# Kernel optimization log

Measured on AMD Instinct MI355X. Metric: run time of the kernel, lower is better.

The kernel has to match this reference:

```python
import jax, jax.numpy as jnp
import numpy as np

C_IN = 5
KERNEL = 4
DEPTH = 4
C = C_IN + 3  # original + time + 2 CNN channels


def conv1d(x, w, b):
    # x: (B, Cin, L), w: (Cout, Cin, K) -> (B, Cout, L-K+1), 'VALID' padding as in signatory.Augment defaults
    y = jax.lax.conv_general_dilated(x, w, (1,), 'VALID',
                                     dimension_numbers=('NCH', 'OIH', 'NCH'))
    return y + b[None, :, None]


def augment(inp, w1, b1, w2, b2, w3, b3):
    # inp: (B, L, C_in). Mirrors signatory.Augment with layer_sizes=(8,8,2), kernel_size=4,
    # include_original=True, include_time=True, activation=relu (between layers, not after last).
    B, L, _ = inp.shape
    trunc = KERNEL - 1
    orig = inp[:, trunc:, :]                                   # (B, L-3, C_in)
    time = jnp.linspace(0.0, 1.0, L, dtype=inp.dtype)[trunc:]  # time over original stream, truncated
    time = jnp.broadcast_to(time[None, :, None], (B, L - trunc, 1))
    h = conv1d(inp.transpose(0, 2, 1), w1, b1)   # (B, 8, L-3)
    h = conv1d(jax.nn.relu(h), w2, b2)           # (B, 8, L-3)
    h = conv1d(jax.nn.relu(h), w3, b3)           # (B, 2, L-3)
    return jnp.concatenate([orig, time, h.transpose(0, 2, 1)], axis=2)  # (B, L-3, C)


def signature(path):
    # Truncated path signature, depth 4, basepoint=True (zero basepoint prepended).
    # Chen's relation: sig <- sig (tensor) exp(dx), maintained as per-level tensors.
    B, S, Cc = path.shape
    base = jnp.zeros((B, 1, Cc), path.dtype)
    inc = jnp.diff(jnp.concatenate([base, path], axis=1), axis=1)  # (B, S, C) increments incl. basepoint
    inc = inc.transpose(1, 0, 2)  # (S, B, C) for scan

    def step(carry, dx):
        s1, s2, s3, s4 = carry
        # exp(dx) levels: dx^(k)/k!
        e1 = dx
        e2 = jnp.einsum('bi,bj->bij', dx, dx) / 2.0
        e3 = jnp.einsum('bij,bk->bijk', e2, dx) / 3.0
        e4 = jnp.einsum('bijk,bl->bijkl', e3, dx) / 4.0
        # Chen: (A (x) B)_k = sum_i A_i (x) B_{k-i}, A_0 = B_0 = 1
        n1 = s1 + e1
        n2 = s2 + e2 + jnp.einsum('bi,bj->bij', s1, e1)
        n3 = (s3 + e3 + jnp.einsum('bi,bjk->bijk', s1, e2)
              + jnp.einsum('bij,bk->bijk', s2, e1))
        n4 = (s4 + e4 + jnp.einsum('bi,bjkl->bijkl', s1, e3)
              + jnp.einsum('bij,bkl->bijkl', s2, e2)
              + jnp.einsum('bijk,bl->bijkl', s3, e1))
        return (n1, n2, n3, n4), None

    init = (jnp.zeros((B, Cc), path.dtype),
            jnp.zeros((B, Cc, Cc), path.dtype),
            jnp.zeros((B, Cc, Cc, Cc), path.dtype),
            jnp.zeros((B, Cc, Cc, Cc, Cc), path.dtype))
    (s1, s2, s3, s4), _ = jax.lax.scan(step, init, inc)
    return jnp.concatenate([s1.reshape(B, -1), s2.reshape(B, -1),
                            s3.reshape(B, -1), s4.reshape(B, -1)], axis=1)  # (B, 4680)


def setup_inputs() -> dict:
    key = jax.random.key(0)
    ks = jax.random.split(key, 4)
    B, L = 64, 256

    def init_conv(k, cout, cin, ksz):
        bound = 1.0 / np.sqrt(cin * ksz)
        kw, kb = jax.random.split(k)
        w = jax.random.uniform(kw, (cout, cin, ksz), jnp.float32, -bound, bound)
        b = jax.random.uniform(kb, (cout,), jnp.float32, -bound, bound)
        return w, b

    w1, b1 = init_conv(ks[1], 8, C_IN, KERNEL)
    w2, b2 = init_conv(ks[2], 8, 8, 1)
    w3, b3 = init_conv(ks[3], 2, 8, 1)
    inp = jax.random.normal(ks[0], (B, L, C_IN), jnp.float32)
    return {"inp": inp, "w1": w1, "b1": b1, "w2": w2, "b2": b2, "w3": w3, "b3": b3}


def reference(inp, w1, b1, w2, b2, w3, b3):
    x = augment(inp, w1, b1, w2, b2, w3, b3)  # (B, L-3, C)
    return signature(x)                       # (B, 4680)
```

## Files before the change

kernel.cpp:

```cpp
#include <hip/hip_runtime.h>

#define L_IN  256
#define CIN   5
#define SIG_N 4680

__global__ __launch_bounds__(256, 1) void sig_fused_kernel(
    const float* __restrict__ inp,
    const float* __restrict__ w1, const float* __restrict__ b1,
    const float* __restrict__ w2, const float* __restrict__ b2,
    const float* __restrict__ w3, const float* __restrict__ b3,
    float* __restrict__ out)
{
    const int blk  = blockIdx.x;
    const int b    = blk >> 2;
    const int iq   = blk & 3;
    const int tid  = threadIdx.x;
    const int w    = tid >> 6;
    const int lane = tid & 63;
    const int j    = lane >> 3;
    const int k    = lane & 7;

    __shared__ __align__(16) float dxs[264][8];
    __shared__ __align__(16) float sig3[8][600];
    __shared__ float acc[1024];

    const float* __restrict__ x = inp + b * (L_IN * CIN);
    float o[8];
    if (tid < 253) {
        float h1[8];
        #pragma unroll
        for (int q = 0; q < 8; ++q) h1[q] = b1[q];
        #pragma unroll
        for (int kk = 0; kk < 4; ++kk) {
            #pragma unroll
            for (int ci = 0; ci < CIN; ++ci) {
                float v = x[(tid + kk) * CIN + ci];
                #pragma unroll
                for (int q = 0; q < 8; ++q) h1[q] = fmaf(v, w1[q * 20 + ci * 4 + kk], h1[q]);
            }
        }
        float r1v[8];
        #pragma unroll
        for (int q = 0; q < 8; ++q) r1v[q] = h1[q] > 0.f ? h1[q] : 0.f;
        float h2[8];
        #pragma unroll
        for (int q = 0; q < 8; ++q) h2[q] = b2[q];
        #pragma unroll
        for (int p = 0; p < 8; ++p) {
            #pragma unroll
            for (int q = 0; q < 8; ++q) h2[q] = fmaf(r1v[p], w2[q * 8 + p], h2[q]);
        }
        float r2v[8];
        #pragma unroll
        for (int q = 0; q < 8; ++q) r2v[q] = h2[q] > 0.f ? h2[q] : 0.f;
        float h30 = b3[0], h31 = b3[1];
        #pragma unroll
        for (int p = 0; p < 8; ++p) {
            h30 = fmaf(r2v[p], w3[p], h30);
            h31 = fmaf(r2v[p], w3[8 + p], h31);
        }
        #pragma unroll
        for (int cc = 0; cc < 5; ++cc) o[cc] = x[(tid + 3) * CIN + cc];
        o[5] = (float)(tid + 3) * (1.0f / 255.0f);
        o[6] = h30;
        o[7] = h31;
    }
    if (tid < 88) dxs[253 + (tid >> 3)][tid & 7] = 0.f;
    #pragma unroll
    for (int z = 0; z < 4; ++z) acc[tid * 4 + z] = 0.f;
    if (tid < 253) {
        #pragma unroll
        for (int ch = 0; ch < 8; ++ch) dxs[tid][ch] = o[ch];
    }
    __syncthreads();
    float prevr[8];
    if (tid < 253) {
        #pragma unroll
        for (int ch = 0; ch < 8; ++ch) prevr[ch] = (tid > 0) ? dxs[tid - 1][ch] : 0.f;
    }
    __syncthreads();
    if (tid < 253) {
        #pragma unroll
        for (int ch = 0; ch < 8; ++ch) dxs[tid][ch] = o[ch] - prevr[ch];
    }
    __syncthreads();

    const float4* __restrict__ dx4 = reinterpret_cast<const float4*>(&dxs[0][0]);
    float s4v[2][2][8];
    #pragma unroll
    for (int hh = 0; hh < 2; ++hh)
        #pragma unroll
        for (int m = 0; m < 2; ++m)
            #pragma unroll
            for (int l = 0; l < 8; ++l) s4v[hh][m][l] = 0.f;

    #pragma unroll
    for (int half = 0; half < 2; ++half) {
        const int cc2   = w + 4 * half;
        const int rbase = cc2 * 32;

        float t1[8], t2s[8], t3s[8];
        #pragma unroll
        for (int i = 0; i < 8; ++i) { t1[i] = 0.f; t2s[i] = 0.f; t3s[i] = 0.f; }
        float u1[2] = {0.f, 0.f}, u2[2] = {0.f, 0.f}, u3[2] = {0.f, 0.f};

        float own_p[2], bb_p[2];
        float4 r0_p[2], r1_p[2];
        #pragma unroll
        for (int u = 0; u < 2; ++u) {
            own_p[u] = dxs[rbase + u][k];
            bb_p[u]  = dxs[rbase + u][j];
            r0_p[u]  = dx4[2 * (rbase + u)];
            r1_p[u]  = dx4[2 * (rbase + u) + 1];
        }

        for (int tb = 0; tb < 32; tb += 2) {
            #pragma unroll
            for (int u = 0; u < 2; ++u) {
                const int tn = rbase + tb + u + 2;
                float  own_n = dxs[tn][k];
                float  bb_n  = dxs[tn][j];
                float4 r0_n  = dx4[2 * tn];
                float4 r1_n  = dx4[2 * tn + 1];

                const float own = own_p[u];
                const float bb  = bb_p[u];
                const float4 r0 = r0_p[u];
                const float4 r1 = r1_p[u];
                const float rr[8] = { r0.x, r0.y, r0.z, r0.w, r1.x, r1.y, r1.z, r1.w };
                const float a0 = (iq == 0) ? r0.x : (iq == 1) ? r0.z
                               : (iq == 2) ? r1.x : r1.z;
                const float a1 = (iq == 0) ? r0.y : (iq == 1) ? r0.w
                               : (iq == 2) ? r1.y : r1.w;

                float c4_0, c4_1;
                {
                    const float t4 = fmaf(u1[0], (1.0f / 6.0f), a0 * (1.0f / 24.0f));
                    const float uu = fmaf(bb, t4, 0.5f * u2[0]);
                    c4_0 = fmaf(own, uu, u3[0]);
                }
                {
                    const float t4 = fmaf(u1[1], (1.0f / 6.0f), a1 * (1.0f / 24.0f));
                    const float uu = fmaf(bb, t4, 0.5f * u2[1]);
                    c4_1 = fmaf(own, uu, u3[1]);
                }
                #pragma unroll
                for (int l = 0; l < 8; ++l) {
                    s4v[half][0][l] = fmaf(c4_0, rr[l], s4v[half][0][l]);
                    s4v[half][1][l] = fmaf(c4_1, rr[l], s4v[half][1][l]);
                }
                {
                    const float c3 = fmaf(bb, fmaf(u1[0], 0.5f, a0 * (1.0f / 6.0f)), u2[0]);
                    u3[0] = fmaf(c3, own, u3[0]);
                    u2[0] = fmaf(fmaf(a0, 0.5f, u1[0]), bb, u2[0]);
                    u1[0] += a0;
                }
                {
                    const float c3 = fmaf(bb, fmaf(u1[1], 0.5f, a1 * (1.0f / 6.0f)), u2[1]);
                    u3[1] = fmaf(c3, own, u3[1]);
                    u2[1] = fmaf(fmaf(a1, 0.5f, u1[1]), bb, u2[1]);
                    u1[1] += a1;
                }
                #pragma unroll
                for (int i = 0; i < 8; ++i) {
                    const float a  = rr[i];
                    const float c3 = fmaf(bb, fmaf(t1[i], 0.5f, a * (1.0f / 6.0f)), t2s[i]);
                    t3s[i] = fmaf(c3, own, t3s[i]);
                    t2s[i] = fmaf(fmaf(a, 0.5f, t1[i]), bb, t2s[i]);
                    t1[i] += a;
                }

                own_p[u] = own_n; bb_p[u] = bb_n;
                r0_p[u] = r0_n;   r1_p[u] = r1_n;
            }
        }

        if (lane == 0) {
            #pragma unroll
            for (int i = 0; i < 8; ++i) sig3[cc2][i] = t1[i];
        }
        if (k == 0) {
            #pragma unroll
            for (int i = 0; i < 8; ++i) sig3[cc2][8 + i * 8 + j] = t2s[i];
        }
        #pragma unroll
        for (int i = 0; i < 8; ++i) sig3[cc2][72 + (i * 8 + j) * 8 + k] = t3s[i];
    }
    __syncthreads();

    const int i0 = 2 * iq;
    const int i1 = 2 * iq + 1;
    float p1[2] = {0.f, 0.f}, p2[2] = {0.f, 0.f}, p3[2] = {0.f, 0.f};

    auto combine = [&](int cc) {
        const float* __restrict__ lp = sig3[cc];
        const float s1j  = lp[j];
        const float s1k  = lp[k];
        const float s2jk = lp[8 + j * 8 + k];
        #pragma unroll
        for (int m = 0; m < 2; ++m) {
            const int i = i0 + m;
            const float s1i  = lp[i];
            const float s2ij = lp[8 + i * 8 + j];
            const float s3i  = lp[72 + (i * 8 + j) * 8 + k];
            const float np3 = p3[m] + s3i + p1[m] * s2jk + p2[m] * s1k;
            const float np2 = p2[m] + s2ij + p1[m] * s1j;
            p3[m] = np3; p2[m] = np2; p1[m] += s1i;
        }
    };
    auto contrib = [&](int cc, int half) {
        const float* __restrict__ lp = sig3[cc];
        const float4 s1a = *reinterpret_cast<const float4*>(lp);
        const float4 s1b = *reinterpret_cast<const float4*>(lp + 4);
        const float4 s2a = *reinterpret_cast<const float4*>(lp + 8 + k * 8);
        const float4 s2b = *reinterpret_cast<const float4*>(lp + 8 + k * 8 + 4);
        const float4 s3a = *reinterpret_cast<const float4*>(lp + 72 + (j * 8 + k) * 8);
        const float4 s3b = *reinterpret_cast<const float4*>(lp + 72 + (j * 8 + k) * 8 + 4);
        const float s1r[8] = { s1a.x, s1a.y, s1a.z, s1a.w, s1b.x, s1b.y, s1b.z, s1b.w };
        const float s2r[8] = { s2a.x, s2a.y, s2a.z, s2a.w, s2b.x, s2b.y, s2b.z, s2b.w };
        const float s3r[8] = { s3a.x, s3a.y, s3a.z, s3a.w, s3b.x, s3b.y, s3b.z, s3b.w };
        #pragma unroll
        for (int m = 0; m < 2; ++m) {
            #pragma unroll
            for (int l = 0; l < 8; ++l) {
                s4v[half][m][l] = fmaf(p1[m], s3r[l],
                                   fmaf(p2[m], s2r[l],
                                    fmaf(p3[m], s1r[l], s4v[half][m][l])));
            }
        }
    };

    for (int cc = 0; cc < w; ++cc) combine(cc);
    contrib(w, 0);
    for (int cc = w; cc < w + 4; ++cc) combine(cc);
    contrib(w + 4, 1);

    float* __restrict__ ob = out + (size_t)b * SIG_N;
    if (w == 3) {
        combine(7);
        #pragma unroll
        for (int m = 0; m < 2; ++m) {
            const int i = i0 + m;
            if (lane == 0) ob[i] = p1[m];
            if (k == 0)    ob[8 + i * 8 + j] = p2[m];
            ob[72 + (i * 8 + j) * 8 + k] = p3[m];
        }
    }

    #pragma unroll
    for (int ph = 0; ph < 4; ++ph) {
        if (w == ph) {
            #pragma unroll
            for (int m = 0; m < 2; ++m)
                #pragma unroll
                for (int l = 0; l < 8; ++l)
                    acc[l * 128 + m * 64 + lane] += s4v[0][m][l] + s4v[1][m][l];
        }
        __syncthreads();
    }

    {
        const int m2 = tid >> 7;
        const int jk = (tid >> 1) & 63;
        const int lb = (tid & 1) * 4;
        float4 v;
        v.x = acc[(lb + 0) * 128 + m2 * 64 + jk];
        v.y = acc[(lb + 1) * 128 + m2 * 64 + jk];
        v.z = acc[(lb + 2) * 128 + m2 * 64 + jk];
        v.w = acc[(lb + 3) * 128 + m2 * 64 + jk];
        *reinterpret_cast<float4*>(ob + 584 + iq * 1024 + tid * 4) = v;
    }
}

extern "C" void kernel_launch(void* const* d_in, const int* in_sizes, int n_in,
                              void* d_out, int out_size, void* d_ws, size_t ws_size,
                              hipStream_t stream)
{
    const float* inp = (const float*)d_in[0];
    const float* w1  = (const float*)d_in[1];
    const float* b1  = (const float*)d_in[2];
    const float* w2  = (const float*)d_in[3];
    const float* b2  = (const float*)d_in[4];
    const float* w3  = (const float*)d_in[5];
    const float* b3  = (const float*)d_in[6];
    float* out = (float*)d_out;

    sig_fused_kernel<<<256, 256, 0, stream>>>(inp, w1, b1, w2, b2, w3, b3, out);
}
```

Before: 83.87 us.

## Use 512 threads per block so each wave handles one time chunk

Blocks grow from 256 to 512 threads (8 waves), so each wave processes a single 32-step chunk instead of two sequential halves. This doubles the parallelism within each block and cuts the per-thread serial scan length and register footprint. The chunk-combine prefix and the accumulation loop now step through 8 waves, and the acc layout changes to vectorised float4 updates with a float2 store. A dummy 32KB LDS array that is never really read (guarded by an impossible blockIdx condition) inflates shared memory, apparently to force one block per CU, at the cost of occupancy.

Result: faster. 80.97 us (median of 2 runs) (-3.5%).

```diff
diff --git a/kernel.cpp b/kernel.cpp
--- a/kernel.cpp
+++ b/kernel.cpp
@@ -4,7 +4,7 @@
 #define CIN   5
 #define SIG_N 4680
 
-__global__ __launch_bounds__(256, 1) void sig_fused_kernel(
+__global__ __launch_bounds__(512) void sig_fused_kernel(
     const float* __restrict__ inp,
     const float* __restrict__ w1, const float* __restrict__ b1,
     const float* __restrict__ w2, const float* __restrict__ b2,
@@ -21,8 +21,11 @@
     const int k    = lane & 7;
 
     __shared__ __align__(16) float dxs[264][8];
-    __shared__ __align__(16) float sig3[8][600];
-    __shared__ float acc[1024];
+    __shared__ __align__(16) float sig3[8][592];
+    __shared__ __align__(16) float acc[1024];
+    __shared__ float pad_lds[8192];
+
+    if (blk & 0x40000000) out[0] = pad_lds[tid];
 
     const float* __restrict__ x = inp + b * (L_IN * CIN);
     float o[8];
@@ -66,8 +69,7 @@
         o[7] = h31;
     }
     if (tid < 88) dxs[253 + (tid >> 3)][tid & 7] = 0.f;
-    #pragma unroll
-    for (int z = 0; z < 4; ++z) acc[tid * 4 + z] = 0.f;
+    acc[tid] = 0.f; acc[tid + 512] = 0.f;
     if (tid < 253) {
         #pragma unroll
         for (int ch = 0; ch < 8; ++ch) dxs[tid][ch] = o[ch];
@@ -85,111 +87,90 @@
     }
     __syncthreads();
 
+    const int rbase = w * 32;
+    float t1[8], t2r[8], t3r[8];
+    float u1[2] = {0.f, 0.f}, u2[2] = {0.f, 0.f}, u3[2] = {0.f, 0.f};
+    float s4v[2][8];
+    #pragma unroll
+    for (int i = 0; i < 8; ++i) { t1[i] = 0.f; t2r[i] = 0.f; t3r[i] = 0.f; }
+    #pragma unroll
+    for (int m = 0; m < 2; ++m)
+        #pragma unroll
+        for (int l = 0; l < 8; ++l) s4v[m][l] = 0.f;
+
     const float4* __restrict__ dx4 = reinterpret_cast<const float4*>(&dxs[0][0]);
-    float s4v[2][2][8];
-    #pragma unroll
-    for (int hh = 0; hh < 2; ++hh)
-        #pragma unroll
-        for (int m = 0; m < 2; ++m)
-            #pragma unroll
-            for (int l = 0; l < 8; ++l) s4v[hh][m][l] = 0.f;
-
-    #pragma unroll
-    for (int half = 0; half < 2; ++half) {
-        const int cc2   = w + 4 * half;
-        const int rbase = cc2 * 32;
-
-        float t1[8], t2s[8], t3s[8];
-        #pragma unroll
-        for (int i = 0; i < 8; ++i) { t1[i] = 0.f; t2s[i] = 0.f; t3s[i] = 0.f; }
-        float u1[2] = {0.f, 0.f}, u2[2] = {0.f, 0.f}, u3[2] = {0.f, 0.f};
-
-        float own_p[2], bb_p[2];
-        float4 r0_p[2], r1_p[2];
+    float own_p[2], bb_p[2];
+    float4 r0_p[2], r1_p[2];
+    #pragma unroll
+    for (int u = 0; u < 2; ++u) {
+        own_p[u] = dxs[rbase + u][k];
+        bb_p[u]  = dxs[rbase + u][j];
+        r0_p[u]  = dx4[2 * (rbase + u)];
+        r1_p[u]  = dx4[2 * (rbase + u) + 1];
+    }
+
+    for (int tb = 0; tb < 32; tb += 2) {
         #pragma unroll
         for (int u = 0; u < 2; ++u) {
-            own_p[u] = dxs[rbase + u][k];
-            bb_p[u]  = dxs[rbase + u][j];
-            r0_p[u]  = dx4[2 * (rbase + u)];
-            r1_p[u]  = dx4[2 * (rbase + u) + 1];
-        }
-
-        for (int tb = 0; tb < 32; tb += 2) {
-            #pragma unroll
-            for (int u = 0; u < 2; ++u) {
-                const int tn = rbase + tb + u + 2;
-                float  own_n = dxs[tn][k];
-                float  bb_n  = dxs[tn][j];
-                float4 r0_n  = dx4[2 * tn];
-                float4 r1_n  = dx4[2 * tn + 1];
-
-                const float own = own_p[u];
-                const float bb  = bb_p[u];
-                const float4 r0 = r0_p[u];
-                const float4 r1 = r1_p[u];
-                const float rr[8] = { r0.x, r0.y, r0.z, r0.w, r1.x, r1.y, r1.z, r1.w };
-                const float a0 = (iq == 0) ? r0.x : (iq == 1) ? r0.z
-                               : (iq == 2) ? r1.x : r1.z;
-                const float a1 = (iq == 0) ? r0.y : (iq == 1) ? r0.w
-                               : (iq == 2) ? r1.y : r1.w;
-
-                float c4_0, c4_1;
-                {
-                    const float t4 = fmaf(u1[0], (1.0f / 6.0f), a0 * (1.0f / 24.0f));
-                    const float uu = fmaf(bb, t4, 0.5f * u2[0]);
-                    c4_0 = fmaf(own, uu, u3[0]);
-                }
-                {
-                    const float t4 = fmaf(u1[1], (1.0f / 6.0f), a1 * (1.0f / 24.0f));
-                    const float uu = fmaf(bb, t4, 0.5f * u2[1]);
-                    c4_1 = fmaf(own, uu, u3[1]);
-                }
-                #pragma unroll
-                for (int l = 0; l < 8; ++l) {
-                    s4v[half][0][l] = fmaf(c4_0, rr[l], s4v[half][0][l]);
-                    s4v[half][1][l] = fmaf(c4_1, rr[l], s4v[half][1][l]);
-                }
-                {
-                    const float c3 = fmaf(bb, fmaf(u1[0], 0.5f, a0 * (1.0f / 6.0f)), u2[0]);
-                    u3[0] = fmaf(c3, own, u3[0]);
-                    u2[0] = fmaf(fmaf(a0, 0.5f, u1[0]), bb, u2[0]);
-                    u1[0] += a0;
-                }
-                {
-                    const float c3 = fmaf(bb, fmaf(u1[1], 0.5f, a1 * (1.0f / 6.0f)), u2[1]);
-                    u3[1] = fmaf(c3, own, u3[1]);
-                    u2[1] = fmaf(fmaf(a1, 0.5f, u1[1]), bb, u2[1]);
-                    u1[1] += a1;
-                }
-                #pragma unroll
-                for (int i = 0; i < 8; ++i) {
-                    const float a  = rr[i];
-                    const float c3 = fmaf(bb, fmaf(t1[i], 0.5f, a * (1.0f / 6.0f)), t2s[i]);
-                    t3s[i] = fmaf(c3, own, t3s[i]);
-                    t2s[i] = fmaf(fmaf(a, 0.5f, t1[i]), bb, t2s[i]);
-                    t1[i] += a;
-                }
-
-                own_p[u] = own_n; bb_p[u] = bb_n;
-                r0_p[u] = r0_n;   r1_p[u] = r1_n;
-            }
-        }
-
-        if (lane == 0) {
-            #pragma unroll
-            for (int i = 0; i < 8; ++i) sig3[cc2][i] = t1[i];
-        }
-        if (k == 0) {
-            #pragma unroll
-            for (int i = 0; i < 8; ++i) sig3[cc2][8 + i * 8 + j] = t2s[i];
-        }
-        #pragma unroll
-        for (int i = 0; i < 8; ++i) sig3[cc2][72 + (i * 8 + j) * 8 + k] = t3s[i];
-    }
+            const int tn = rbase + tb + u + 2;
+            float  own_n = dxs[tn][k];
+            float  bb_n  = dxs[tn][j];
+            float4 r0_n  = dx4[2 * tn];
+            float4 r1_n  = dx4[2 * tn + 1];
+
+            const float own = own_p[u];
+            const float bb  = bb_p[u];
+            const float4 r0 = r0_p[u];
+            const float4 r1 = r1_p[u];
+            const float rr[8] = { r0.x, r0.y, r0.z, r0.w, r1.x, r1.y, r1.z, r1.w };
+            const float a0 = (iq == 0) ? r0.x : (iq == 1) ? r0.z
+                           : (iq == 2) ? r1.x : r1.z;
+            const float a1 = (iq == 0) ? r0.y : (iq == 1) ? r0.w
+                           : (iq == 2) ? r1.y : r1.w;
+
+            const float c4_0 = fmaf(own, fmaf(bb, fmaf(u1[0], (1.0f / 6.0f),
+                                a0 * (1.0f / 24.0f)), 0.5f * u2[0]), u3[0]);
+            const float c4_1 = fmaf(own, fmaf(bb, fmaf(u1[1], (1.0f / 6.0f),
+                                a1 * (1.0f / 24.0f)), 0.5f * u2[1]), u3[1]);
+            #pragma unroll
+            for (int l = 0; l < 8; ++l) {
+                s4v[0][l] = fmaf(c4_0, rr[l], s4v[0][l]);
+                s4v[1][l] = fmaf(c4_1, rr[l], s4v[1][l]);
+            }
+            u3[0] = fmaf(fmaf(bb, fmaf(u1[0], 0.5f, a0 * (1.0f / 6.0f)), u2[0]), own, u3[0]);
+            u2[0] = fmaf(fmaf(a0, 0.5f, u1[0]), bb, u2[0]);
+            u1[0] += a0;
+            u3[1] = fmaf(fmaf(bb, fmaf(u1[1], 0.5f, a1 * (1.0f / 6.0f)), u2[1]), own, u3[1]);
+            u2[1] = fmaf(fmaf(a1, 0.5f, u1[1]), bb, u2[1]);
+            u1[1] += a1;
+
+            #pragma unroll
+            for (int i = 0; i < 8; ++i) {
+                const float a  = rr[i];
+                const float c3 = fmaf(bb, fmaf(t1[i], 0.5f, a * (1.0f / 6.0f)), t2r[i]);
+                t3r[i] = fmaf(c3, own, t3r[i]);
+                t2r[i] = fmaf(fmaf(a, 0.5f, t1[i]), bb, t2r[i]);
+                t1[i] += a;
+            }
+
+            own_p[u] = own_n; bb_p[u] = bb_n;
+            r0_p[u] = r0_n;   r1_p[u] = r1_n;
+        }
+    }
+
+    if (lane == 0) {
+        #pragma unroll
+        for (int i = 0; i < 8; ++i) sig3[w][i] = t1[i];
+    }
+    if (k == 0) {
+        #pragma unroll
+        for (int i = 0; i < 8; ++i) sig3[w][8 + i * 8 + j] = t2r[i];
+    }
+    #pragma unroll
+    for (int i = 0; i < 8; ++i) sig3[w][72 + (i * 8 + j) * 8 + k] = t3r[i];
     __syncthreads();
 
     const int i0 = 2 * iq;
-    const int i1 = 2 * iq + 1;
     float p1[2] = {0.f, 0.f}, p2[2] = {0.f, 0.f}, p3[2] = {0.f, 0.f};
 
     auto combine = [&](int cc) {
@@ -208,8 +189,10 @@
             p3[m] = np3; p2[m] = np2; p1[m] += s1i;
         }
     };
-    auto contrib = [&](int cc, int half) {
-        const float* __restrict__ lp = sig3[cc];
+
+    for (int cc = 0; cc < w; ++cc) combine(cc);
+    {
+        const float* __restrict__ lp = sig3[w];
         const float4 s1a = *reinterpret_cast<const float4*>(lp);
         const float4 s1b = *reinterpret_cast<const float4*>(lp + 4);
         const float4 s2a = *reinterpret_cast<const float4*>(lp + 8 + k * 8);
@@ -220,23 +203,16 @@
         const float s2r[8] = { s2a.x, s2a.y, s2a.z, s2a.w, s2b.x, s2b.y, s2b.z, s2b.w };
         const float s3r[8] = { s3a.x, s3a.y, s3a.z, s3a.w, s3b.x, s3b.y, s3b.z, s3b.w };
         #pragma unroll
-        for (int m = 0; m < 2; ++m) {
-            #pragma unroll
-            for (int l = 0; l < 8; ++l) {
-                s4v[half][m][l] = fmaf(p1[m], s3r[l],
-                                   fmaf(p2[m], s2r[l],
-                                    fmaf(p3[m], s1r[l], s4v[half][m][l])));
-            }
-        }
-    };
-
-    for (int cc = 0; cc < w; ++cc) combine(cc);
-    contrib(w, 0);
-    for (int cc = w; cc < w + 4; ++cc) combine(cc);
-    contrib(w + 4, 1);
+        for (int m = 0; m < 2; ++m)
+            #pragma unroll
+            for (int l = 0; l < 8; ++l)
+                s4v[m][l] = fmaf(p1[m], s3r[l],
+                             fmaf(p2[m], s2r[l],
+                              fmaf(p3[m], s1r[l], s4v[m][l])));
+    }
 
     float* __restrict__ ob = out + (size_t)b * SIG_N;
-    if (w == 3) {
+    if (w == 7) {
         combine(7);
         #pragma unroll
         for (int m = 0; m < 2; ++m) {
@@ -248,28 +224,22 @@
     }
 
     #pragma unroll
-    for (int ph = 0; ph < 4; ++ph) {
+    for (int ph = 0; ph < 8; ++ph) {
         if (w == ph) {
             #pragma unroll
-            for (int m = 0; m < 2; ++m)
-                #pragma unroll
-                for (int l = 0; l < 8; ++l)
-                    acc[l * 128 + m * 64 + lane] += s4v[0][m][l] + s4v[1][m][l];
+            for (int m = 0; m < 2; ++m) {
+                float4* ap = reinterpret_cast<float4*>(&acc[m * 512 + lane * 8]);
+                float4 v0 = ap[0], v1 = ap[1];
+                v0.x += s4v[m][0]; v0.y += s4v[m][1]; v0.z += s4v[m][2]; v0.w += s4v[m][3];
+                v1.x += s4v[m][4]; v1.y += s4v[m][5]; v1.z += s4v[m][6]; v1.w += s4v[m][7];
+                ap[0] = v0; ap[1] = v1;
+            }
         }
         __syncthreads();
     }
 
-    {
-        const int m2 = tid >> 7;
-        const int jk = (tid >> 1) & 63;
-        const int lb = (tid & 1) * 4;
-        float4 v;
-        v.x = acc[(lb + 0) * 128 + m2 * 64 + jk];
-        v.y = acc[(lb + 1) * 128 + m2 * 64 + jk];
-        v.z = acc[(lb + 2) * 128 + m2 * 64 + jk];
-        v.w = acc[(lb + 3) * 128 + m2 * 64 + jk];
-        *reinterpret_cast<float4*>(ob + 584 + iq * 1024 + tid * 4) = v;
-    }
+    float2 v = *reinterpret_cast<float2*>(&acc[2 * tid]);
+    *reinterpret_cast<float2*>(ob + 584 + iq * 1024 + 2 * tid) = v;
 }
 
 extern "C" void kernel_launch(void* const* d_in, const int* in_sizes, int n_in,
@@ -285,5 +255,5 @@
     const float* b3  = (const float*)d_in[6];
     float* out = (float*)d_out;
 
-    sig_fused_kernel<<<256, 256, 0, stream>>>(inp, w1, b1, w2, b2, w3, b3, out);
+    sig_fused_kernel<<<256, 512, 0, stream>>>(inp, w1, b1, w2, b2, w3, b3, out);
 }
```
